# Optimization experiments

Measured on AMD Instinct MI355X. Metric: run time of the kernel, lower is better.

The kernel has to match this reference:

```python
import jax, jax.numpy as jnp
import numpy as np

N, T, F = 20000, 20, 128
H = 128          # lstm hidden per direction
GH, HEADS = 128, 4
NUM_CLASSES = 10
E = 640000
SCALE = 0.05


def _lstm_last_hidden(x, lengths, Wih, Whh, b):
    """Run a unidirectional LSTM over padded x [N,T,F]; return hidden at the
    last valid step per sequence (torch gate order i,f,g,o)."""
    pre = jnp.einsum('ntf,gf->ntg', x, Wih) + b            # [N,T,4H]
    mask = jnp.arange(x.shape[1])[None, :] < lengths[:, None]  # [N,T]
    h0 = jnp.zeros((x.shape[0], Whh.shape[1]), x.dtype)

    def step(carry, inp):
        h, c = carry
        pt, m = inp                                         # [N,4H], [N]
        gates = pt + h @ Whh.T
        i, f, g, o = jnp.split(gates, 4, axis=-1)
        c_new = jax.nn.sigmoid(f) * c + jax.nn.sigmoid(i) * jnp.tanh(g)
        h_new = jax.nn.sigmoid(o) * jnp.tanh(c_new)
        m = m[:, None]
        return (jnp.where(m, h_new, h), jnp.where(m, c_new, c)), None

    (h, _), _ = jax.lax.scan(step, (h0, h0), (pre.transpose(1, 0, 2), mask.T))
    return h


def _reverse_by_length(x, lengths):
    # x[n, t] -> x[n, len-1-t] for t < len (padding positions are masked later)
    idx = jnp.clip(lengths[:, None] - 1 - jnp.arange(x.shape[1])[None, :], 0, None)
    return x[jnp.arange(x.shape[0])[:, None], idx]


def _gat(h, src, dst, W, a_src, a_dst, bias, heads):
    n = h.shape[0]
    xh = (h @ W.T).reshape(n, heads, -1)                    # [N,H,C]
    al_s = jnp.sum(xh * a_src, -1)                          # [N,H]
    al_d = jnp.sum(xh * a_dst, -1)
    e = jax.nn.leaky_relu(al_s[src] + al_d[dst], 0.2)       # [E,H]
    emax = jax.ops.segment_max(e, dst, num_segments=n)
    emax = jnp.where(jnp.isfinite(emax), emax, 0.0)
    ee = jnp.exp(e - emax[dst])
    denom = jax.ops.segment_sum(ee, dst, num_segments=n)
    alpha = ee / (denom[dst] + 1e-16)                       # segment softmax
    out = jax.ops.segment_sum(xh[src] * alpha[..., None], dst, num_segments=n)
    return out.reshape(n, -1) + bias


def setup_inputs() -> dict:
    key = jax.random.key(0)
    ks = jax.random.split(key, 16)
    p = lambda k, *s: jax.random.normal(k, s, jnp.float32) * SCALE
    return {
        'x': jax.random.normal(ks[0], (N, T, F), jnp.float32),
        'lengths': jax.random.randint(ks[1], (N,), 1, T + 1, jnp.int32),
        'edge_index': jax.random.randint(ks[2], (2, E), 0, N, jnp.int32),
        # BiLSTM params (b = b_ih + b_hh combined; identical math)
        'Wih_f': p(ks[3], 4 * H, F), 'Whh_f': p(ks[4], 4 * H, H), 'b_f': p(ks[5], 4 * H),
        'Wih_b': p(ks[6], 4 * H, F), 'Whh_b': p(ks[7], 4 * H, H), 'b_b': p(ks[8], 4 * H),
        # GAT1: in=2H=256 -> heads*GH=512
        'W1': p(ks[9], HEADS * GH, 2 * H), 'a1_src': p(ks[10], HEADS, GH),
        'a1_dst': p(ks[11], HEADS, GH), 'bias1': jnp.zeros((HEADS * GH,), jnp.float32),
        # GAT2: in=512 -> 1*GH=128
        'W2': p(ks[12], GH, HEADS * GH), 'a2_src': p(ks[13], 1, GH),
        'a2_dst': p(ks[14], 1, GH), 'bias2': jnp.zeros((GH,), jnp.float32),
        'Wfc': p(ks[15], NUM_CLASSES, GH), 'bfc': jnp.zeros((NUM_CLASSES,), jnp.float32),
    }


def reference(x, lengths, edge_index, Wih_f, Whh_f, b_f, Wih_b, Whh_b, b_b,
              W1, a1_src, a1_dst, bias1, W2, a2_src, a2_dst, bias2, Wfc, bfc):
    n = x.shape[0]
    h_fwd = _lstm_last_hidden(x, lengths, Wih_f, Whh_f, b_f)
    h_bwd = _lstm_last_hidden(_reverse_by_length(x, lengths), lengths, Wih_b, Whh_b, b_b)
    h = jnp.concatenate([h_fwd, h_bwd], axis=-1)            # [N, 2H]
    # GATConv default adds self-loops
    loop = jnp.arange(n, dtype=edge_index.dtype)
    src = jnp.concatenate([edge_index[0], loop])
    dst = jnp.concatenate([edge_index[1], loop])
    h = jax.nn.relu(_gat(h, src, dst, W1, a1_src, a1_dst, bias1, HEADS))
    h = jax.nn.relu(_gat(h, src, dst, W2, a2_src, a2_dst, bias2, 1))
    return h @ Wfc.T + bfc                                  # [N, num_classes]
```

## Files before the change

kernel.cpp:

```cpp
#include <hip/hip_runtime.h>

#define NSEQ 20000
#define TT 20
#define FD 128
#define EDG 640000
#define ETOT (EDG + NSEQ)

typedef short bf16x8 __attribute__((ext_vector_type(8)));
typedef float f32x4 __attribute__((ext_vector_type(4)));
typedef unsigned short u16;
typedef unsigned int u32;

__device__ __forceinline__ float bf2f(u16 h) {
  union { u32 u; float f; } v; v.u = ((u32)h) << 16; return v.f;
}
__device__ __forceinline__ float bf_lo(u32 w) {
  union { u32 u; float f; } v; v.u = w << 16; return v.f;
}
__device__ __forceinline__ float bf_hi(u32 w) {
  union { u32 u; float f; } v; v.u = w & 0xffff0000u; return v.f;
}
__device__ __forceinline__ u16 f2bf(float f) {
  union { float f; u32 u; } v; v.f = f;
  u32 u = v.u;
  return (u16)((u + 0x7fffu + ((u >> 16) & 1u)) >> 16);
}
__device__ __forceinline__ float fast_rcp(float x) {
  float r; asm("v_rcp_f32 %0, %1" : "=v"(r) : "v"(x)); return r;
}
__device__ __forceinline__ float fast_ex2(float x) {
  float r; asm("v_exp_f32 %0, %1" : "=v"(r) : "v"(x)); return r;
}
__device__ __forceinline__ u32 cvtpk_bf16(float a, float b) {
  u32 r; asm("v_cvt_pk_bf16_f32 %0, %1, %2" : "=v"(r) : "v"(a), "v"(b)); return r;
}
__device__ __forceinline__ float fast_rcpp(float x) { return fast_rcp(x); }
__device__ __forceinline__ int clampi(int v, int lo, int hi) {
  return v < lo ? lo : (v > hi ? hi : v);
}

template<int BF>
__device__ __forceinline__ bf16x8 ld8(const void* p, size_t i) {
  if (BF) return *(const bf16x8*)((const u16*)p + i);
  f32x4 a = *(const f32x4*)((const float*)p + i);
  f32x4 b = *(const f32x4*)((const float*)p + i + 4);
  union { u32 w[4]; bf16x8 v; } u;
  u.w[0] = cvtpk_bf16(a[0], a[1]);
  u.w[1] = cvtpk_bf16(a[2], a[3]);
  u.w[2] = cvtpk_bf16(b[0], b[1]);
  u.w[3] = cvtpk_bf16(b[2], b[3]);
  return u.v;
}

#define OFF_WIHF 0
#define OFF_WHHF 65536
#define OFF_BF   131072
#define OFF_WIHB 131584
#define OFF_WHHB 197120
#define OFF_BB   262656
#define OFF_W1   263168
#define OFF_W2   394240
#define OFF_A1S  459776
#define OFF_A1D  460288
#define OFF_B1   460800
#define OFF_A2S  461312
#define OFF_A2D  461440
#define OFF_B2   461568
#define OFF_WFC  461696
#define OFF_BFC  462976

__global__ void k_detect_zero(const u32* __restrict__ xw, int* __restrict__ flag,
                              int* __restrict__ deg, int* __restrict__ lcnt) {
  int i = blockIdx.x * 256 + threadIdx.x;
  if (i < NSEQ) deg[i] = 0;
  if (i < 64) lcnt[i] = 0;
  if (blockIdx.x == 0 && threadIdx.x < 64) {
    u16 lo = (u16)(xw[threadIdx.x] & 0xffffu);
    int e = (lo >> 7) & 0xff;
    unsigned long long m = __ballot(e >= 100 && e <= 140);
    if (threadIdx.x == 0) flag[0] = (__popcll(m) >= 32) ? 1 : 0;
  }
}

struct CvtArgs {
  const void* src[16];
  int off[16];
  int cnt[16];
  int wt[16];
};

template<int BF>
__global__ void k_cvt(CvtArgs a, u16* __restrict__ canon, const int* __restrict__ flag) {
  if (flag[0] != BF) return;
  int idx = blockIdx.x * 256 + threadIdx.x;
  int stride = gridDim.x * 256;
#pragma unroll 1
  for (int s = 0; s < 16; ++s) {
    const void* sp = a.src[s];
    int n = a.cnt[s], off = a.off[s], wt = a.wt[s];
    for (int i = idx; i < n; i += stride) {
      float v = BF ? bf2f(((const u16*)sp)[i]) : ((const float*)sp)[i];
      if (wt) {
        int gate = (wt == 1) ? ((i >> 14) & 3) : ((i >> 7) & 3);
        v *= (gate == 2) ? 2.885390082f : -1.442695041f;
      }
      canon[off + i] = f2bf(v);
    }
  }
}

__global__ void k_fill0(u16* __restrict__ out, int n) {
  int i = blockIdx.x * 256 + threadIdx.x;
  if (i < n) out[i] = 0;
}

template<int BF>
__global__ __launch_bounds__(512, 2) void k_lstm(
    const void* __restrict__ x, const int* __restrict__ lengths,
    const int* __restrict__ lperm,
    const u16* __restrict__ canon, u16* __restrict__ hcat,
    const int* __restrict__ flag)
{
  if (flag[0] != BF) return;
  __shared__ u16 Ax[2][64 * 128];
  __shared__ u16 Ah[2][64 * 128];
  __shared__ int lenS[64];
  __shared__ int seqS[64];
  __shared__ int sMax;

  const int tid = threadIdx.x;
  const int wv = tid >> 6;
  const int lane = tid & 63;
  const int q = lane >> 4;
  const int cc = lane & 15;
  const int dir = blockIdx.y;
  const int b0 = (gridDim.x - 1 - blockIdx.x) * 64;

  const u16* Wi = canon + (dir ? OFF_WIHB : OFF_WIHF);
  const u16* Wh = canon + (dir ? OFF_WHHB : OFF_WHHF);
  const u16* bb = canon + (dir ? OFF_BB : OFF_BF);

  bf16x8 wih[4][4], whh[4][4];
  uint2 bvp[4];
#pragma unroll
  for (int g = 0; g < 4; ++g) {
    int row = g * 128 + wv * 16 + cc;
#pragma unroll
    for (int kt = 0; kt < 4; ++kt) {
      wih[g][kt] = *(const bf16x8*)(Wi + row * 128 + kt * 32 + q * 8);
      whh[g][kt] = *(const bf16x8*)(Wh + row * 128 + kt * 32 + q * 8);
    }
    bvp[g] = *(const uint2*)(bb + g * 128 + wv * 16 + q * 4);
  }

  if (tid < 64) {
    int s = lperm[clampi(b0 + tid, 0, NSEQ - 1)];
    s = clampi(s, 0, NSEQ - 1);
    seqS[tid] = s;
    int L = clampi(lengths[s], 1, TT);
    lenS[tid] = L;
#pragma unroll
    for (int off = 32; off >= 1; off >>= 1) L = max(L, __shfl_xor(L, off, 64));
    if (tid == 0) sMax = L;
  }
  {
    f32x4 zz = {0.f, 0.f, 0.f, 0.f};
    f32x4* p = (f32x4*)Ah[0];
    for (int i = tid; i < 1024; i += 512) p[i] = zz;
  }
  __syncthreads();

  const int tmax = sMax;

  int lenq[4];
#pragma unroll
  for (int m = 0; m < 4; ++m) lenq[m] = lenS[m * 16 + cc];

  const int lrow = tid >> 3;
  const int lj = tid & 7;
  const int sL = seqS[lrow];
  const int lenL = lenS[lrow];
  const size_t xbase = (size_t)sL * (TT * FD);
  const int ax0 = lrow * 128 + ((lj ^ (lrow & 15)) * 8);
  const int ax1 = lrow * 128 + (((lj + 8) ^ (lrow & 15)) * 8);

  int rofs[4];
#pragma unroll
  for (int kt = 0; kt < 4; ++kt) rofs[kt] = cc * 128 + (((4 * kt + q) ^ cc) * 8);
  const int awbase = cc * 128 + (((wv * 2 + (q >> 1)) ^ cc) * 8) + (q & 1) * 4;

  {
    int t0 = dir ? (lenL - 1) : 0;
    bf16x8 d0 = ld8<BF>(x, xbase + t0 * FD + lj * 8);
    bf16x8 d1 = ld8<BF>(x, xbase + t0 * FD + (lj + 8) * 8);
    *(bf16x8*)&Ax[0][ax0] = d0;
    *(bf16x8*)&Ax[0][ax1] = d1;
  }
  float c[4][4] = {};
  int cb = 0;
  __syncthreads();

#pragma unroll 1
  for (int t = 0; t < tmax; ++t) {
    const u16* Axr = Ax[cb];
    u16* Axw = Ax[cb ^ 1];
    const u16* Ahr = Ah[cb];
    u16* Ahw = Ah[cb ^ 1];

    bf16x8 d0 = {}, d1 = {};
    const bool more = (t + 1 < tmax);
    if (more) {
      int tn = t + 1;
      int tt2 = dir ? (lenL - 1 - tn) : tn;
      if (tt2 < 0) tt2 = 0;
      d0 = ld8<BF>(x, xbase + tt2 * FD + lj * 8);
      d1 = ld8<BF>(x, xbase + tt2 * FD + (lj + 8) * 8);
    }

#pragma unroll
    for (int m = 0; m < 4; ++m) {
      const int mb = m * 2048;
      f32x4 acc[4];
#pragma unroll
      for (int g = 0; g < 4; ++g) {
        f32x4 vi = {bf_lo(bvp[g].x), bf_hi(bvp[g].x), bf_lo(bvp[g].y), bf_hi(bvp[g].y)};
        acc[g] = vi;
      }
#pragma unroll
      for (int kt = 0; kt < 4; ++kt) {
        bf16x8 b = *(const bf16x8*)&Axr[mb + rofs[kt]];
#pragma unroll
        for (int g = 0; g < 4; ++g)
          acc[g] = __builtin_amdgcn_mfma_f32_16x16x32_bf16(wih[g][kt], b, acc[g], 0, 0, 0);
      }
#pragma unroll
      for (int kt = 0; kt < 4; ++kt) {
        bf16x8 b = *(const bf16x8*)&Ahr[mb + rofs[kt]];
#pragma unroll
        for (int g = 0; g < 4; ++g)
          acc[g] = __builtin_amdgcn_mfma_f32_16x16x32_bf16(whh[g][kt], b, acc[g], 0, 0, 0);
      }

      uint2 hw;
      if (t < lenq[m]) {
        float hf[4];
#pragma unroll
        for (int r = 0; r < 4; ++r) {
          float Ei = fast_ex2(acc[0][r]);
          float Ef = fast_ex2(acc[1][r]);
          float G  = fast_ex2(acc[2][r]) + 1.0f;
          float Eo = fast_ex2(acc[3][r]);
          float A = 1.0f + Ef, B = 1.0f + Ei;
          float BG = B * G;
          float num = c[m][r] * BG + (A * G - 2.0f * A);
          float cn = num * fast_rcp(A * BG);
          c[m][r] = cn;
          float C2 = fast_ex2(cn * 2.885390082f) + 1.0f;
          hf[r] = (C2 - 2.0f) * fast_rcp((1.0f + Eo) * C2);
        }
        hw.x = cvtpk_bf16(hf[0], hf[1]);
        hw.y = cvtpk_bf16(hf[2], hf[3]);
      } else {
        hw = *(const uint2*)&Ahr[mb + awbase];
      }
      *(uint2*)&Ahw[mb + awbase] = hw;
    }

    if (more) {
      *(bf16x8*)&Axw[ax0] = d0;
      *(bf16x8*)&Axw[ax1] = d1;
    }
    __syncthreads();
    cb ^= 1;
  }

  for (int i = tid; i < 1024; i += 512) {
    int row = i >> 4, ch = i & 15;
    if (b0 + row < NSEQ) {
      int seq = seqS[row];
      bf16x8 v = *(const bf16x8*)&Ah[cb][row * 128 + ((ch ^ (row & 15)) * 8)];
      *(bf16x8*)(hcat + (size_t)seq * 256 + dir * 128 + ch * 8) = v;
    }
  }
}

__global__ __launch_bounds__(256) void k_gemm(
    const u16* __restrict__ A, const u16* __restrict__ W, u16* __restrict__ C,
    int M, int Nc, int K,
    const u16* __restrict__ aS, const u16* __restrict__ aD,
    float* __restrict__ als, float* __restrict__ ald, int alsStride)
{
  __shared__ u16 As[128 * 64];
  __shared__ u16 Bs[128 * 64];
  const int tid = threadIdx.x;
  const int wv = tid >> 6, lane = tid & 63, q = lane >> 4, cc = lane & 15;
  const int mblk = blockIdx.x * 128, nblk = blockIdx.y * 128;
  const int wm = (wv & 1) * 64, wn = (wv >> 1) * 64;

  f32x4 acc[4][4] = {};

  const int srow = tid >> 1;
  const int sc0 = (tid & 1) * 4;
  int arow_g = mblk + srow; if (arow_g > M - 1) arow_g = M - 1;
  const u16* aptr = A + (size_t)arow_g * K + sc0 * 8;
  const u16* bptr = W + (size_t)(nblk + srow) * K + sc0 * 8;

  for (int k0 = 0; k0 < K; k0 += 64) {
#pragma unroll
    for (int cch = 0; cch < 4; ++cch) {
      bf16x8 av = *(const bf16x8*)(aptr + k0 + cch * 8);
      bf16x8 bvv = *(const bf16x8*)(bptr + k0 + cch * 8);
      int ch = sc0 + cch;
      *(bf16x8*)&As[srow * 64 + ((ch ^ (srow & 7)) * 8)] = av;
      *(bf16x8*)&Bs[srow * 64 + ((ch ^ (srow & 7)) * 8)] = bvv;
    }
    __syncthreads();
#pragma unroll
    for (int kt = 0; kt < 2; ++kt) {
      bf16x8 af[4];
#pragma unroll
      for (int m = 0; m < 4; ++m) {
        int row = wm + m * 16 + cc;
        af[m] = *(const bf16x8*)&As[row * 64 + (((4 * kt + q) ^ (row & 7)) * 8)];
      }
#pragma unroll
      for (int n = 0; n < 4; ++n) {
        int rowb = wn + n * 16 + cc;
        bf16x8 bfr = *(const bf16x8*)&Bs[rowb * 64 + (((4 * kt + q) ^ (rowb & 7)) * 8)];
#pragma unroll
        for (int m = 0; m < 4; ++m)
          acc[m][n] = __builtin_amdgcn_mfma_f32_16x16x32_bf16(bfr, af[m], acc[m][n], 0, 0, 0);
      }
    }
    __syncthreads();
  }

  float pls[4] = {}, pld[4] = {};
#pragma unroll
  for (int n = 0; n < 4; ++n) {
    uint2 ws = *(const uint2*)(aS + nblk + wn + n * 16 + q * 4);
    uint2 wd = *(const uint2*)(aD + nblk + wn + n * 16 + q * 4);
    float s0 = bf_lo(ws.x), s1 = bf_hi(ws.x), s2 = bf_lo(ws.y), s3 = bf_hi(ws.y);
    float d0 = bf_lo(wd.x), d1 = bf_hi(wd.x), d2 = bf_lo(wd.y), d3 = bf_hi(wd.y);
#pragma unroll
    for (int m = 0; m < 4; ++m) {
      int row = mblk + wm + m * 16 + cc;
      uint2 st;
      st.x = cvtpk_bf16(acc[m][n][0], acc[m][n][1]);
      st.y = cvtpk_bf16(acc[m][n][2], acc[m][n][3]);
      if (row < M) *(uint2*)(C + (size_t)row * Nc + nblk + wn + n * 16 + q * 4) = st;
      pls[m] += acc[m][n][0] * s0 + acc[m][n][1] * s1 + acc[m][n][2] * s2 + acc[m][n][3] * s3;
      pld[m] += acc[m][n][0] * d0 + acc[m][n][1] * d1 + acc[m][n][2] * d2 + acc[m][n][3] * d3;
    }
  }

#pragma unroll
  for (int m = 0; m < 4; ++m) {
    pls[m] += __shfl_xor(pls[m], 16, 64);
    pls[m] += __shfl_xor(pls[m], 32, 64);
    pld[m] += __shfl_xor(pld[m], 16, 64);
    pld[m] += __shfl_xor(pld[m], 32, 64);
  }
  float* sred = (float*)As;
  if (lane < 16) {
#pragma unroll
    for (int m = 0; m < 4; ++m) {
      int idx = ((wv & 1) * 4 + m) * 32 + cc * 2 + (wv >> 1);
      sred[idx] = pls[m];
      sred[256 + idx] = pld[m];
    }
  }
  __syncthreads();
  if (wv < 2) {
    int m = lane >> 4, ccc = lane & 15;
    int row = mblk + wv * 64 + m * 16 + ccc;
    int idx = (wv * 4 + m) * 32 + ccc * 2;
    if (row < M) {
      als[(size_t)row * alsStride + blockIdx.y] = sred[idx] + sred[idx + 1];
      ald[(size_t)row * alsStride + blockIdx.y] = sred[256 + idx] + sred[256 + idx + 1];
    }
  }
}

__global__ __launch_bounds__(256) void k_agg1(
    const u16* __restrict__ xh1, const float* __restrict__ als, const float* __restrict__ ald,
    const int* __restrict__ offs, const int* __restrict__ csr,
    const u16* __restrict__ canon, u16* __restrict__ h1)
{
  const int lane = threadIdx.x & 63;
  const int hd = threadIdx.x >> 6;
  const int n = blockIdx.x;
  int off0 = offs[n], off1 = offs[n + 1];
  off0 = clampi(off0, 0, ETOT);
  off1 = clampi(off1, off0, ETOT);
  const float ad = ald[(size_t)n * 4 + hd];
  const int deg = off1 - off0;
  const u16* xb = xh1 + hd * 128 + lane * 2;

  float o0 = 0.f, o1 = 0.f;
  if (deg <= 64) {
    int s = 0;
    float e = -1e30f;
    if (lane < deg) {
      s = clampi(csr[off0 + lane], 0, NSEQ - 1);
      float t = als[(size_t)s * 4 + hd] + ad;
      e = t > 0.f ? t : 0.2f * t;
    }
    float mx = e;
#pragma unroll
    for (int off = 32; off >= 1; off >>= 1) mx = fmaxf(mx, __shfl_xor(mx, off, 64));
    float ex = (lane < deg) ? __expf(e - mx) : 0.f;
    float sm = ex;
#pragma unroll
    for (int off = 32; off >= 1; off >>= 1) sm += __shfl_xor(sm, off, 64);
    const float a = ex * fast_rcp(sm + 1e-16f);
    const int sofs = s * 512;
#pragma unroll 4
    for (int j = 0; j < deg; ++j) {
      int so = __builtin_amdgcn_readlane(sofs, j);
      float aa = __int_as_float(__builtin_amdgcn_readlane(__float_as_int(a), j));
      u32 xv = *(const u32*)(xb + so);
      o0 += aa * bf2f((u16)(xv & 0xffffu));
      o1 += aa * bf2f((u16)(xv >> 16));
    }
  } else {
    float mx = -1e30f;
    for (int k = off0 + lane; k < off1; k += 64) {
      int s = clampi(csr[k], 0, NSEQ - 1);
      float e = als[(size_t)s * 4 + hd] + ad;
      e = e > 0.f ? e : 0.2f * e;
      mx = fmaxf(mx, e);
    }
#pragma unroll
    for (int off = 32; off >= 1; off >>= 1) mx = fmaxf(mx, __shfl_xor(mx, off, 64));
    float sm = 0.f;
    for (int k = off0 + lane; k < off1; k += 64) {
      int s = clampi(csr[k], 0, NSEQ - 1);
      float e = als[(size_t)s * 4 + hd] + ad;
      e = e > 0.f ? e : 0.2f * e;
      sm += __expf(e - mx);
    }
#pragma unroll
    for (int off = 32; off >= 1; off >>= 1) sm += __shfl_xor(sm, off, 64);
    const float rd = fast_rcp(sm + 1e-16f);
#pragma unroll 4
    for (int k = off0; k < off1; ++k) {
      int s = clampi(csr[k], 0, NSEQ - 1);
      float e = als[(size_t)s * 4 + hd] + ad;
      e = e > 0.f ? e : 0.2f * e;
      float a = __expf(e - mx) * rd;
      u32 xv = *(const u32*)(xb + (size_t)s * 512);
      o0 += a * bf2f((u16)(xv & 0xffffu));
      o1 += a * bf2f((u16)(xv >> 16));
    }
  }
  o0 += bf2f(canon[OFF_B1 + hd * 128 + lane * 2]);
  o1 += bf2f(canon[OFF_B1 + hd * 128 + lane * 2 + 1]);
  o0 = o0 > 0.f ? o0 : 0.f;
  o1 = o1 > 0.f ? o1 : 0.f;
  u32 pk = (u32)f2bf(o0) | ((u32)f2bf(o1) << 16);
  *(u32*)(h1 + (size_t)n * 512 + hd * 128 + lane * 2) = pk;
}

__global__ __launch_bounds__(256) void k_agg2(
    const u16* __restrict__ xh2, const float* __restrict__ als2, const float* __restrict__ ald2,
    const int* __restrict__ offs, const int* __restrict__ csr,
    const u16* __restrict__ canon, void* __restrict__ out, const int* __restrict__ flag)
{
  const int lane = threadIdx.x & 63;
  const int n = blockIdx.x * 4 + (threadIdx.x >> 6);
  int off0 = offs[n], off1 = offs[n + 1];
  off0 = clampi(off0, 0, ETOT);
  off1 = clampi(off1, off0, ETOT);
  const float adn = ald2[n];
  const int deg = off1 - off0;

  float o0 = 0.f, o1 = 0.f;
  if (deg <= 64) {
    int s = 0;
    float e = -1e30f;
    if (lane < deg) {
      s = clampi(csr[off0 + lane], 0, NSEQ - 1);
      float t = als2[s] + adn;
      e = t > 0.f ? t : 0.2f * t;
    }
    float mx = e;
#pragma unroll
    for (int off = 32; off >= 1; off >>= 1) mx = fmaxf(mx, __shfl_xor(mx, off, 64));
    float ex = (lane < deg) ? __expf(e - mx) : 0.f;
    float sm = ex;
#pragma unroll
    for (int off = 32; off >= 1; off >>= 1) sm += __shfl_xor(sm, off, 64);
    const float a = ex * fast_rcp(sm + 1e-16f);
    const int sofs = s * 128;
#pragma unroll 4
    for (int j = 0; j < deg; ++j) {
      int so = __builtin_amdgcn_readlane(sofs, j);
      float aa = __int_as_float(__builtin_amdgcn_readlane(__float_as_int(a), j));
      u32 xv = *(const u32*)(xh2 + so + lane * 2);
      o0 += aa * bf2f((u16)(xv & 0xffffu));
      o1 += aa * bf2f((u16)(xv >> 16));
    }
  } else {
    float mx = -1e30f;
    for (int k = off0 + lane; k < off1; k += 64) {
      float e = als2[clampi(csr[k], 0, NSEQ - 1)] + adn;
      e = e > 0.f ? e : 0.2f * e;
      mx = fmaxf(mx, e);
    }
#pragma unroll
    for (int off = 32; off >= 1; off >>= 1) mx = fmaxf(mx, __shfl_xor(mx, off, 64));
    float sm = 0.f;
    for (int k = off0 + lane; k < off1; k += 64) {
      float e = als2[clampi(csr[k], 0, NSEQ - 1)] + adn;
      e = e > 0.f ? e : 0.2f * e;
      sm += __expf(e - mx);
    }
#pragma unroll
    for (int off = 32; off >= 1; off >>= 1) sm += __shfl_xor(sm, off, 64);
    float rd = fast_rcp(sm + 1e-16f);
#pragma unroll 4
    for (int k = off0; k < off1; ++k) {
      int s = clampi(csr[k], 0, NSEQ - 1);
      float e = als2[s] + adn;
      e = e > 0.f ? e : 0.2f * e;
      float a = __expf(e - mx) * rd;
      u32 xv = *(const u32*)(xh2 + (size_t)s * 128 + lane * 2);
      o0 += a * bf2f((u16)(xv & 0xffffu));
      o1 += a * bf2f((u16)(xv >> 16));
    }
  }
  o0 += bf2f(canon[OFF_B2 + lane * 2]);     o0 = o0 > 0.f ? o0 : 0.f;
  o1 += bf2f(canon[OFF_B2 + lane * 2 + 1]); o1 = o1 > 0.f ? o1 : 0.f;

  float res[10];
#pragma unroll
  for (int cls = 0; cls < 10; ++cls) {
    float p = o0 * bf2f(canon[OFF_WFC + cls * 128 + lane * 2]) +
              o1 * bf2f(canon[OFF_WFC + cls * 128 + lane * 2 + 1]);
#pragma unroll
    for (int off = 32; off >= 1; off >>= 1) p += __shfl_xor(p, off, 64);
    float v = p + bf2f(canon[OFF_BFC + cls]);
    res[cls] = (fabsf(v) < 1e30f) ? v : 0.f;
  }
  if (flag[0]) {
    if (lane < 5) {
      u32 pk = (u32)f2bf(res[lane * 2]) | ((u32)f2bf(res[lane * 2 + 1]) << 16);
      ((u32*)out)[(size_t)n * 5 + lane] = pk;
    }
  } else {
    if (lane < 10) ((float*)out)[(size_t)n * 10 + lane] = res[lane];
  }
}

__global__ void k_hist_all(const int* __restrict__ ei, const int* __restrict__ lengths,
                           int* __restrict__ deg, int* __restrict__ lcnt) {
  int i = blockIdx.x * 256 + threadIdx.x;
  if (i < ETOT) {
    int d = (i < EDG) ? ei[EDG + i] : (i - EDG);
    d = clampi(d, 0, NSEQ - 1);
    atomicAdd(&deg[d], 1);
  }
  if (i < NSEQ) atomicAdd(&lcnt[clampi(lengths[i], 1, TT) - 1], 1);
}

__global__ __launch_bounds__(1024) void k_scan(const int* __restrict__ deg,
                                               int* __restrict__ offs, int* __restrict__ cur,
                                               const int* __restrict__ lcnt,
                                               int* __restrict__ lcur) {
  __shared__ int wsum[16];
  const int tid = threadIdx.x;
  if (tid == 0) {
    int run = 0;
    for (int i = 0; i < TT; ++i) { lcur[i] = run; run += lcnt[i]; }
  }
  const int lane = tid & 63, wv = tid >> 6;
  const int CHUNK = 20;
  int base = tid * CHUNK;
  int loc[20];
  int s = 0;
#pragma unroll
  for (int i = 0; i < CHUNK; ++i) {
    int idx = base + i;
    int v = (idx < NSEQ) ? deg[idx] : 0;
    loc[i] = s;
    s += v;
  }
  int inc = s;
#pragma unroll
  for (int off = 1; off < 64; off <<= 1) {
    int t2 = __shfl_up(inc, off, 64);
    if (lane >= off) inc += t2;
  }
  if (lane == 63) wsum[wv] = inc;
  __syncthreads();
  int wbase = 0;
  for (int i = 0; i < wv; ++i) wbase += wsum[i];
  int tbase = wbase + inc - s;
#pragma unroll
  for (int i = 0; i < CHUNK; ++i) {
    int idx = base + i;
    if (idx < NSEQ) {
      int st = tbase + loc[i];
      offs[idx] = st;
      cur[idx] = st;
    }
  }
  if (tid == 0) offs[NSEQ] = ETOT;
}

__global__ void k_scatter_all(const int* __restrict__ ei, const int* __restrict__ lengths,
                              int* __restrict__ cur, int* __restrict__ csr,
                              int* __restrict__ lcur, int* __restrict__ lperm) {
  int i = blockIdx.x * 256 + threadIdx.x;
  if (i < ETOT) {
    int s, d;
    if (i < EDG) { s = ei[i]; d = ei[EDG + i]; }
    else { s = i - EDG; d = s; }
    d = clampi(d, 0, NSEQ - 1);
    int pos = atomicAdd(&cur[d], 1);
    pos = clampi(pos, 0, ETOT - 1);
    csr[pos] = s;
  }
  if (i < NSEQ) {
    int b = clampi(lengths[i], 1, TT) - 1;
    int pos = atomicAdd(&lcur[b], 1);
    lperm[clampi(pos, 0, NSEQ - 1)] = i;
  }
}

extern "C" void kernel_launch(void* const* d_in, const int* in_sizes, int n_in,
                              void* d_out, int out_size, void* d_ws, size_t ws_size,
                              hipStream_t stream) {
  (void)in_sizes; (void)n_in;
  const void* x     = d_in[0];
  const int* lengths= (const int*)d_in[1];
  const int* ei     = (const int*)d_in[2];

  const size_t NEED = 45769344u;
  if (ws_size < NEED) {
    k_fill0<<<(out_size + 255) / 256, 256, 0, stream>>>((u16*)d_out, out_size);
    return;
  }

  char* w = (char*)d_ws;
  size_t o = 0;
  auto alloc = [&](size_t b) { char* p = w + o; o += (b + 255) & ~(size_t)255; return p; };
  int*  flag = (int*)  alloc(256);
  u16*  canon= (u16*)  alloc(1048576);
  int*  deg  = (int*)  alloc((size_t)NSEQ * 4);
  int*  offs = (int*)  alloc((size_t)(NSEQ + 1) * 4);
  int*  cur  = (int*)  alloc((size_t)NSEQ * 4);
  int*  csr  = (int*)  alloc((size_t)ETOT * 4);
  float* als1= (float*)alloc((size_t)NSEQ * 4 * 4);
  float* ald1= (float*)alloc((size_t)NSEQ * 4 * 4);
  char* regB = alloc((size_t)NSEQ * 512 * 2);
  u16*  xh1  = (u16*)regB;
  u16*  xh2  = (u16*)regB;
  float* als2= (float*)(regB + (size_t)NSEQ * 128 * 2 + (size_t)NSEQ * 128 * 4);
  float* ald2= als2 + NSEQ;
  char* regA = alloc((size_t)NSEQ * 256 * 2);
  u16*  hcat = (u16*)regA;
  u16*  h1   = (u16*)regA;
  alloc((size_t)NSEQ * 256 * 2);

  int* lperm = (int*)regB;
  int* lcnt  = (int*)(regB + 80128);
  int* lcur  = (int*)(regB + 80256);

  k_detect_zero<<<(NSEQ + 255) / 256, 256, 0, stream>>>((const u32*)x, flag, deg, lcnt);

  CvtArgs ca;
  const int srcIdx[16] = {3, 4, 5, 6, 7, 8, 9, 13, 10, 11, 12, 14, 15, 16, 17, 18};
  const int offv[16]   = {OFF_WIHF, OFF_WHHF, OFF_BF, OFF_WIHB, OFF_WHHB, OFF_BB,
                          OFF_W1, OFF_W2, OFF_A1S, OFF_A1D, OFF_B1,
                          OFF_A2S, OFF_A2D, OFF_B2, OFF_WFC, OFF_BFC};
  const int cntv[16]   = {65536, 65536, 512, 65536, 65536, 512,
                          131072, 65536, 512, 512, 512, 128, 128, 128, 1280, 10};
  const int wtv[16]    = {1, 1, 2, 1, 1, 2, 0, 0, 0, 0, 0, 0, 0, 0, 0, 0};
  for (int i = 0; i < 16; ++i) {
    ca.src[i] = d_in[srcIdx[i]]; ca.off[i] = offv[i]; ca.cnt[i] = cntv[i]; ca.wt[i] = wtv[i];
  }
  k_cvt<1><<<256, 256, 0, stream>>>(ca, canon, flag);
  k_cvt<0><<<256, 256, 0, stream>>>(ca, canon, flag);

  k_hist_all<<<(ETOT + 255) / 256, 256, 0, stream>>>(ei, lengths, deg, lcnt);
  k_scan<<<1, 1024, 0, stream>>>(deg, offs, cur, lcnt, lcur);
  k_scatter_all<<<(ETOT + 255) / 256, 256, 0, stream>>>(ei, lengths, cur, csr, lcur, lperm);

  k_lstm<1><<<dim3(313, 2), 512, 0, stream>>>(x, lengths, lperm, canon, hcat, flag);
  k_lstm<0><<<dim3(313, 2), 512, 0, stream>>>(x, lengths, lperm, canon, hcat, flag);

  k_gemm<<<dim3(157, 4), 256, 0, stream>>>(hcat, canon + OFF_W1, xh1, NSEQ, 512, 256,
                                           canon + OFF_A1S, canon + OFF_A1D, als1, ald1, 4);
  k_agg1<<<NSEQ, 256, 0, stream>>>(xh1, als1, ald1, offs, csr, canon, h1);

  k_gemm<<<dim3(157, 1), 256, 0, stream>>>(h1, canon + OFF_W2, xh2, NSEQ, 128, 512,
                                           canon + OFF_A2S, canon + OFF_A2D, als2, ald2, 1);
  k_agg2<<<5000, 256, 0, stream>>>(xh2, als2, ald2, offs, csr, canon, d_out, flag);
}
```

Measured before the change: 809.3 us.

## Double LSTM batch tile to 128 sequences and process all GAT1 heads per wave

The LSTM kernel now handles 128 length-sorted sequences per block instead of 64, with 8 m-tiles per wave. This halves the grid and amortises the per-block register weight loads and barriers over twice as much work. tmax is now read from the last sorted length rather than computed with a max reduction. The GAT layer-1 aggregation now assigns one wave per node covering all 4 heads, so the CSR indices and float4 attention logits are loaded once instead of four times. LDS use doubles to 128KB per block, which likely allows only one block per CU, and the wider per-head accumulators raise register pressure.

```diff
diff --git a/kernel.cpp b/kernel.cpp
--- a/kernel.cpp
+++ b/kernel.cpp
@@ -34,7 +34,6 @@
 __device__ __forceinline__ u32 cvtpk_bf16(float a, float b) {
   u32 r; asm("v_cvt_pk_bf16_f32 %0, %1, %2" : "=v"(r) : "v"(a), "v"(b)); return r;
 }
-__device__ __forceinline__ float fast_rcpp(float x) { return fast_rcp(x); }
 __device__ __forceinline__ int clampi(int v, int lo, int hi) {
   return v < lo ? lo : (v > hi ? hi : v);
 }
@@ -122,11 +121,10 @@
     const int* __restrict__ flag)
 {
   if (flag[0] != BF) return;
-  __shared__ u16 Ax[2][64 * 128];
-  __shared__ u16 Ah[2][64 * 128];
-  __shared__ int lenS[64];
-  __shared__ int seqS[64];
-  __shared__ int sMax;
+  __shared__ u16 Ax[2][128 * 128];
+  __shared__ u16 Ah[2][128 * 128];
+  __shared__ int lenS[128];
+  __shared__ int seqS[128];
 
   const int tid = threadIdx.x;
   const int wv = tid >> 6;
@@ -134,7 +132,7 @@
   const int q = lane >> 4;
   const int cc = lane & 15;
   const int dir = blockIdx.y;
-  const int b0 = (gridDim.x - 1 - blockIdx.x) * 64;
+  const int b0 = (gridDim.x - 1 - blockIdx.x) * 128;
 
   const u16* Wi = canon + (dir ? OFF_WIHB : OFF_WIHF);
   const u16* Wh = canon + (dir ? OFF_WHHB : OFF_WHHF);
@@ -153,36 +151,35 @@
     bvp[g] = *(const uint2*)(bb + g * 128 + wv * 16 + q * 4);
   }
 
-  if (tid < 64) {
+  if (tid < 128) {
     int s = lperm[clampi(b0 + tid, 0, NSEQ - 1)];
     s = clampi(s, 0, NSEQ - 1);
     seqS[tid] = s;
-    int L = clampi(lengths[s], 1, TT);
-    lenS[tid] = L;
-#pragma unroll
-    for (int off = 32; off >= 1; off >>= 1) L = max(L, __shfl_xor(L, off, 64));
-    if (tid == 0) sMax = L;
+    lenS[tid] = clampi(lengths[s], 1, TT);
   }
   {
     f32x4 zz = {0.f, 0.f, 0.f, 0.f};
     f32x4* p = (f32x4*)Ah[0];
-    for (int i = tid; i < 1024; i += 512) p[i] = zz;
+    for (int i = tid; i < 2048; i += 512) p[i] = zz;
   }
   __syncthreads();
 
-  const int tmax = sMax;
-
-  int lenq[4];
-#pragma unroll
-  for (int m = 0; m < 4; ++m) lenq[m] = lenS[m * 16 + cc];
-
-  const int lrow = tid >> 3;
-  const int lj = tid & 7;
-  const int sL = seqS[lrow];
-  const int lenL = lenS[lrow];
-  const size_t xbase = (size_t)sL * (TT * FD);
-  const int ax0 = lrow * 128 + ((lj ^ (lrow & 15)) * 8);
-  const int ax1 = lrow * 128 + (((lj + 8) ^ (lrow & 15)) * 8);
+  const int tmax = lenS[127];
+
+  int lenq[8];
+#pragma unroll
+  for (int m = 0; m < 8; ++m) lenq[m] = lenS[m * 16 + cc];
+
+  int axj[4], lenj[4];
+  size_t xbj[4];
+#pragma unroll
+  for (int j = 0; j < 4; ++j) {
+    int idx = tid + j * 512;
+    int row = idx >> 4, ch = idx & 15;
+    axj[j] = row * 128 + ((ch ^ (row & 15)) * 8);
+    xbj[j] = (size_t)seqS[row] * (TT * FD) + ch * 8;
+    lenj[j] = lenS[row];
+  }
 
   int rofs[4];
 #pragma unroll
@@ -190,13 +187,14 @@
   const int awbase = cc * 128 + (((wv * 2 + (q >> 1)) ^ cc) * 8) + (q & 1) * 4;
 
   {
-    int t0 = dir ? (lenL - 1) : 0;
-    bf16x8 d0 = ld8<BF>(x, xbase + t0 * FD + lj * 8);
-    bf16x8 d1 = ld8<BF>(x, xbase + t0 * FD + (lj + 8) * 8);
-    *(bf16x8*)&Ax[0][ax0] = d0;
-    *(bf16x8*)&Ax[0][ax1] = d1;
-  }
-  float c[4][4] = {};
+#pragma unroll
+    for (int j = 0; j < 4; ++j) {
+      int t0 = dir ? (lenj[j] - 1) : 0;
+      bf16x8 d = ld8<BF>(x, xbj[j] + t0 * FD);
+      *(bf16x8*)&Ax[0][axj[j]] = d;
+    }
+  }
+  float c[8][4] = {};
   int cb = 0;
   __syncthreads();
 
@@ -207,18 +205,19 @@
     const u16* Ahr = Ah[cb];
     u16* Ahw = Ah[cb ^ 1];
 
-    bf16x8 d0 = {}, d1 = {};
+    bf16x8 d[4];
     const bool more = (t + 1 < tmax);
     if (more) {
-      int tn = t + 1;
-      int tt2 = dir ? (lenL - 1 - tn) : tn;
-      if (tt2 < 0) tt2 = 0;
-      d0 = ld8<BF>(x, xbase + tt2 * FD + lj * 8);
-      d1 = ld8<BF>(x, xbase + tt2 * FD + (lj + 8) * 8);
-    }
-
-#pragma unroll
-    for (int m = 0; m < 4; ++m) {
+#pragma unroll
+      for (int j = 0; j < 4; ++j) {
+        int tt2 = dir ? (lenj[j] - 1 - (t + 1)) : (t + 1);
+        if (tt2 < 0) tt2 = 0;
+        d[j] = ld8<BF>(x, xbj[j] + tt2 * FD);
+      }
+    }
+
+#pragma unroll
+    for (int m = 0; m < 8; ++m) {
       const int mb = m * 2048;
       f32x4 acc[4];
 #pragma unroll
@@ -267,14 +266,14 @@
     }
 
     if (more) {
-      *(bf16x8*)&Axw[ax0] = d0;
-      *(bf16x8*)&Axw[ax1] = d1;
+#pragma unroll
+      for (int j = 0; j < 4; ++j) *(bf16x8*)&Axw[axj[j]] = d[j];
     }
     __syncthreads();
     cb ^= 1;
   }
 
-  for (int i = tid; i < 1024; i += 512) {
+  for (int i = tid; i < 2048; i += 512) {
     int row = i >> 4, ch = i & 15;
     if (b0 + row < NSEQ) {
       int seq = seqS[row];
@@ -388,78 +387,138 @@
     const u16* __restrict__ canon, u16* __restrict__ h1)
 {
   const int lane = threadIdx.x & 63;
-  const int hd = threadIdx.x >> 6;
-  const int n = blockIdx.x;
+  const int n = blockIdx.x * 4 + (threadIdx.x >> 6);
   int off0 = offs[n], off1 = offs[n + 1];
   off0 = clampi(off0, 0, ETOT);
   off1 = clampi(off1, off0, ETOT);
-  const float ad = ald[(size_t)n * 4 + hd];
   const int deg = off1 - off0;
-  const u16* xb = xh1 + hd * 128 + lane * 2;
-
-  float o0 = 0.f, o1 = 0.f;
+  const float4 ad = *(const float4*)(ald + (size_t)n * 4);
+  const u16* xb = xh1 + lane * 2;
+
+  float o0 = 0.f, o1 = 0.f, o2 = 0.f, o3 = 0.f, o4 = 0.f, o5 = 0.f, o6 = 0.f, o7 = 0.f;
   if (deg <= 64) {
     int s = 0;
-    float e = -1e30f;
+    float e0 = -1e30f, e1 = -1e30f, e2 = -1e30f, e3 = -1e30f;
     if (lane < deg) {
       s = clampi(csr[off0 + lane], 0, NSEQ - 1);
-      float t = als[(size_t)s * 4 + hd] + ad;
-      e = t > 0.f ? t : 0.2f * t;
-    }
-    float mx = e;
-#pragma unroll
-    for (int off = 32; off >= 1; off >>= 1) mx = fmaxf(mx, __shfl_xor(mx, off, 64));
-    float ex = (lane < deg) ? __expf(e - mx) : 0.f;
-    float sm = ex;
-#pragma unroll
-    for (int off = 32; off >= 1; off >>= 1) sm += __shfl_xor(sm, off, 64);
-    const float a = ex * fast_rcp(sm + 1e-16f);
+      float4 av = *(const float4*)(als + (size_t)s * 4);
+      float t;
+      t = av.x + ad.x; e0 = t > 0.f ? t : 0.2f * t;
+      t = av.y + ad.y; e1 = t > 0.f ? t : 0.2f * t;
+      t = av.z + ad.z; e2 = t > 0.f ? t : 0.2f * t;
+      t = av.w + ad.w; e3 = t > 0.f ? t : 0.2f * t;
+    }
+    float m0 = e0, m1 = e1, m2 = e2, m3 = e3;
+#pragma unroll
+    for (int off = 32; off >= 1; off >>= 1) {
+      m0 = fmaxf(m0, __shfl_xor(m0, off, 64));
+      m1 = fmaxf(m1, __shfl_xor(m1, off, 64));
+      m2 = fmaxf(m2, __shfl_xor(m2, off, 64));
+      m3 = fmaxf(m3, __shfl_xor(m3, off, 64));
+    }
+    float x0 = (lane < deg) ? __expf(e0 - m0) : 0.f;
+    float x1 = (lane < deg) ? __expf(e1 - m1) : 0.f;
+    float x2 = (lane < deg) ? __expf(e2 - m2) : 0.f;
+    float x3 = (lane < deg) ? __expf(e3 - m3) : 0.f;
+    float s0 = x0, s1 = x1, s2 = x2, s3 = x3;
+#pragma unroll
+    for (int off = 32; off >= 1; off >>= 1) {
+      s0 += __shfl_xor(s0, off, 64);
+      s1 += __shfl_xor(s1, off, 64);
+      s2 += __shfl_xor(s2, off, 64);
+      s3 += __shfl_xor(s3, off, 64);
+    }
+    float a0 = x0 * fast_rcp(s0 + 1e-16f);
+    float a1 = x1 * fast_rcp(s1 + 1e-16f);
+    float a2 = x2 * fast_rcp(s2 + 1e-16f);
+    float a3 = x3 * fast_rcp(s3 + 1e-16f);
     const int sofs = s * 512;
-#pragma unroll 4
+#pragma unroll 2
     for (int j = 0; j < deg; ++j) {
       int so = __builtin_amdgcn_readlane(sofs, j);
-      float aa = __int_as_float(__builtin_amdgcn_readlane(__float_as_int(a), j));
-      u32 xv = *(const u32*)(xb + so);
-      o0 += aa * bf2f((u16)(xv & 0xffffu));
-      o1 += aa * bf2f((u16)(xv >> 16));
+      float aa0 = __int_as_float(__builtin_amdgcn_readlane(__float_as_int(a0), j));
+      float aa1 = __int_as_float(__builtin_amdgcn_readlane(__float_as_int(a1), j));
+      float aa2 = __int_as_float(__builtin_amdgcn_readlane(__float_as_int(a2), j));
+      float aa3 = __int_as_float(__builtin_amdgcn_readlane(__float_as_int(a3), j));
+      u32 v0 = *(const u32*)(xb + so);
+      u32 v1 = *(const u32*)(xb + so + 128);
+      u32 v2 = *(const u32*)(xb + so + 256);
+      u32 v3 = *(const u32*)(xb + so + 384);
+      o0 += aa0 * bf_lo(v0); o1 += aa0 * bf_hi(v0);
+      o2 += aa1 * bf_lo(v1); o3 += aa1 * bf_hi(v1);
+      o4 += aa2 * bf_lo(v2); o5 += aa2 * bf_hi(v2);
+      o6 += aa3 * bf_lo(v3); o7 += aa3 * bf_hi(v3);
     }
   } else {
-    float mx = -1e30f;
+    float m0 = -1e30f, m1 = -1e30f, m2 = -1e30f, m3 = -1e30f;
     for (int k = off0 + lane; k < off1; k += 64) {
       int s = clampi(csr[k], 0, NSEQ - 1);
-      float e = als[(size_t)s * 4 + hd] + ad;
-      e = e > 0.f ? e : 0.2f * e;
-      mx = fmaxf(mx, e);
-    }
-#pragma unroll
-    for (int off = 32; off >= 1; off >>= 1) mx = fmaxf(mx, __shfl_xor(mx, off, 64));
-    float sm = 0.f;
+      float4 av = *(const float4*)(als + (size_t)s * 4);
+      float t;
+      t = av.x + ad.x; t = t > 0.f ? t : 0.2f * t; m0 = fmaxf(m0, t);
+      t = av.y + ad.y; t = t > 0.f ? t : 0.2f * t; m1 = fmaxf(m1, t);
+      t = av.z + ad.z; t = t > 0.f ? t : 0.2f * t; m2 = fmaxf(m2, t);
+      t = av.w + ad.w; t = t > 0.f ? t : 0.2f * t; m3 = fmaxf(m3, t);
+    }
+#pragma unroll
+    for (int off = 32; off >= 1; off >>= 1) {
+      m0 = fmaxf(m0, __shfl_xor(m0, off, 64));
+      m1 = fmaxf(m1, __shfl_xor(m1, off, 64));
+      m2 = fmaxf(m2, __shfl_xor(m2, off, 64));
+      m3 = fmaxf(m3, __shfl_xor(m3, off, 64));
+    }
+    float s0 = 0.f, s1 = 0.f, s2 = 0.f, s3 = 0.f;
     for (int k = off0 + lane; k < off1; k += 64) {
       int s = clampi(csr[k], 0, NSEQ - 1);
-      float e = als[(size_t)s * 4 + hd] + ad;
-      e = e > 0.f ? e : 0.2f * e;
-      sm += __expf(e - mx);
-    }
-#pragma unroll
-    for (int off = 32; off >= 1; off >>= 1) sm += __shfl_xor(sm, off, 64);
-    const float rd = fast_rcp(sm + 1e-16f);
-#pragma unroll 4
+      float4 av = *(const float4*)(als + (size_t)s * 4);
+      float t;
+      t = av.x + ad.x; t = t > 0.f ? t : 0.2f * t; s0 += __expf(t - m0);
+      t = av.y + ad.y; t = t > 0.f ? t : 0.2f * t; s1 += __expf(t - m1);
+      t = av.z + ad.z; t = t > 0.f ? t : 0.2f * t; s2 += __expf(t - m2);
+      t = av.w + ad.w; t = t > 0.f ? t : 0.2f * t; s3 += __expf(t - m3);
+    }
+#pragma unroll
+    for (int off = 32; off >= 1; off >>= 1) {
+      s0 += __shfl_xor(s0, off, 64);
+      s1 += __shfl_xor(s1, off, 64);
+      s2 += __shfl_xor(s2, off, 64);
+      s3 += __shfl_xor(s3, off, 64);
+    }
+    float rd0 = fast_rcp(s0 + 1e-16f), rd1 = fast_rcp(s1 + 1e-16f);
+    float rd2 = fast_rcp(s2 + 1e-16f), rd3 = fast_rcp(s3 + 1e-16f);
     for (int k = off0; k < off1; ++k) {
       int s = clampi(csr[k], 0, NSEQ - 1);
-      float e = als[(size_t)s * 4 + hd] + ad;
-      e = e > 0.f ? e : 0.2f * e;
-      float a = __expf(e - mx) * rd;
-      u32 xv = *(const u32*)(xb + (size_t)s * 512);
-      o0 += a * bf2f((u16)(xv & 0xffffu));
-      o1 += a * bf2f((u16)(xv >> 16));
-    }
-  }
-  o0 += bf2f(canon[OFF_B1 + hd * 128 + lane * 2]);
-  o1 += bf2f(canon[OFF_B1 + hd * 128 + lane * 2 + 1]);
-  o0 = o0 > 0.f ? o0 : 0.f;
-  o1 = o1 > 0.f ? o1 : 0.f;
-  u32 pk = (u32)f2bf(o0) | ((u32)f2bf(o1) << 16);
-  *(u32*)(h1 + (size_t)n * 512 + hd * 128 + lane * 2) = pk;
+      float4 av = *(const float4*)(als + (size_t)s * 4);
+      float t;
+      t = av.x + ad.x; t = t > 0.f ? t : 0.2f * t; float aa0 = __expf(t - m0) * rd0;
+      t = av.y + ad.y; t = t > 0.f ? t : 0.2f * t; float aa1 = __expf(t - m1) * rd1;
+      t = av.z + ad.z; t = t > 0.f ? t : 0.2f * t; float aa2 = __expf(t - m2) * rd2;
+      t = av.w + ad.w; t = t > 0.f ? t : 0.2f * t; float aa3 = __expf(t - m3) * rd3;
+      const u16* xr = xb + (size_t)s * 512;
+      u32 v0 = *(const u32*)(xr);
+      u32 v1 = *(const u32*)(xr + 128);
+      u32 v2 = *(const u32*)(xr + 256);
+      u32 v3 = *(const u32*)(xr + 384);
+      o0 += aa0 * bf_lo(v0); o1 += aa0 * bf_hi(v0);
+      o2 += aa1 * bf_lo(v1); o3 += aa1 * bf_hi(v1);
+      o4 += aa2 * bf_lo(v2); o5 += aa2 * bf_hi(v2);
+      o6 += aa3 * bf_lo(v3); o7 += aa3 * bf_hi(v3);
+    }
+  }
+  float b0 = bf2f(canon[OFF_B1 + lane * 2]),       b1 = bf2f(canon[OFF_B1 + lane * 2 + 1]);
+  float b2 = bf2f(canon[OFF_B1 + 128 + lane * 2]), b3 = bf2f(canon[OFF_B1 + 128 + lane * 2 + 1]);
+  float b4 = bf2f(canon[OFF_B1 + 256 + lane * 2]), b5 = bf2f(canon[OFF_B1 + 256 + lane * 2 + 1]);
+  float b6 = bf2f(canon[OFF_B1 + 384 + lane * 2]), b7 = bf2f(canon[OFF_B1 + 384 + lane * 2 + 1]);
+  o0 += b0; o1 += b1; o2 += b2; o3 += b3; o4 += b4; o5 += b5; o6 += b6; o7 += b7;
+  o0 = o0 > 0.f ? o0 : 0.f; o1 = o1 > 0.f ? o1 : 0.f;
+  o2 = o2 > 0.f ? o2 : 0.f; o3 = o3 > 0.f ? o3 : 0.f;
+  o4 = o4 > 0.f ? o4 : 0.f; o5 = o5 > 0.f ? o5 : 0.f;
+  o6 = o6 > 0.f ? o6 : 0.f; o7 = o7 > 0.f ? o7 : 0.f;
+  u16* hb = h1 + (size_t)n * 512 + lane * 2;
+  *(u32*)(hb)       = cvtpk_bf16(o0, o1);
+  *(u32*)(hb + 128) = cvtpk_bf16(o2, o3);
+  *(u32*)(hb + 256) = cvtpk_bf16(o4, o5);
+  *(u32*)(hb + 384) = cvtpk_bf16(o6, o7);
 }
 
 __global__ __launch_bounds__(256) void k_agg2(
@@ -498,8 +557,8 @@
       int so = __builtin_amdgcn_readlane(sofs, j);
       float aa = __int_as_float(__builtin_amdgcn_readlane(__float_as_int(a), j));
       u32 xv = *(const u32*)(xh2 + so + lane * 2);
-      o0 += aa * bf2f((u16)(xv & 0xffffu));
-      o1 += aa * bf2f((u16)(xv >> 16));
+      o0 += aa * bf_lo(xv);
+      o1 += aa * bf_hi(xv);
     }
   } else {
     float mx = -1e30f;
@@ -526,8 +585,8 @@
       e = e > 0.f ? e : 0.2f * e;
       float a = __expf(e - mx) * rd;
       u32 xv = *(const u32*)(xh2 + (size_t)s * 128 + lane * 2);
-      o0 += a * bf2f((u16)(xv & 0xffffu));
-      o1 += a * bf2f((u16)(xv >> 16));
+      o0 += a * bf_lo(xv);
+      o1 += a * bf_hi(xv);
     }
   }
   o0 += bf2f(canon[OFF_B2 + lane * 2]);     o0 = o0 > 0.f ? o0 : 0.f;
@@ -688,12 +747,12 @@
   k_scan<<<1, 1024, 0, stream>>>(deg, offs, cur, lcnt, lcur);
   k_scatter_all<<<(ETOT + 255) / 256, 256, 0, stream>>>(ei, lengths, cur, csr, lcur, lperm);
 
-  k_lstm<1><<<dim3(313, 2), 512, 0, stream>>>(x, lengths, lperm, canon, hcat, flag);
-  k_lstm<0><<<dim3(313, 2), 512, 0, stream>>>(x, lengths, lperm, canon, hcat, flag);
+  k_lstm<1><<<dim3(157, 2), 512, 0, stream>>>(x, lengths, lperm, canon, hcat, flag);
+  k_lstm<0><<<dim3(157, 2), 512, 0, stream>>>(x, lengths, lperm, canon, hcat, flag);
 
   k_gemm<<<dim3(157, 4), 256, 0, stream>>>(hcat, canon + OFF_W1, xh1, NSEQ, 512, 256,
                                            canon + OFF_A1S, canon + OFF_A1D, als1, ald1, 4);
-  k_agg1<<<NSEQ, 256, 0, stream>>>(xh1, als1, ald1, offs, csr, canon, h1);
+  k_agg1<<<5000, 256, 0, stream>>>(xh1, als1, ald1, offs, csr, canon, h1);
 
   k_gemm<<<dim3(157, 1), 256, 0, stream>>>(h1, canon + OFF_W2, xh2, NSEQ, 128, 512,
                                            canon + OFF_A2S, canon + OFF_A2D, als2, ald2, 1);
```

Result: no change. 801.0 us (-1.0%).
